# Kernel tuning notes

Hardware: AMD Instinct MI355X
Metric: run time of the kernel (lower is better)

The kernel has to match this reference:

```python
import jax, jax.numpy as jnp
import numpy as np

N_NODES = 100000
N_EDGES = 3200000
D = 128


def setup_inputs() -> dict:
    key = jax.random.key(0)
    k1, k2, k3, k4, k5 = jax.random.split(key, 5)
    x = jax.random.normal(k1, (N_NODES, D), dtype=jnp.float32)
    weight = jax.random.normal(k2, (D, D), dtype=jnp.float32) * (1.0 / np.sqrt(D))
    bias = jax.random.normal(k3, (D,), dtype=jnp.float32) * 0.01
    edge_weight = jax.random.uniform(k4, (N_EDGES,), dtype=jnp.float32)
    edge_index = jax.random.randint(k5, (2, N_EDGES), 0, N_NODES, dtype=jnp.int64 if jax.config.jax_enable_x64 else jnp.int32)
    return {"x": x, "weight": weight, "bias": bias,
            "edge_weight": edge_weight, "edge_index": edge_index}


def gcn_conv(x, weight, bias, edge_index, edge_weight):
    # PyG GCNConv defaults: normalize=True, add_self_loops=True (fill=1),
    # flow source_to_target: messages gathered from edge_index[0], scattered to edge_index[1].
    n = x.shape[0]
    src, dst = edge_index[0], edge_index[1]
    loop = jnp.arange(n, dtype=src.dtype)
    src = jnp.concatenate([src, loop])
    dst = jnp.concatenate([dst, loop])
    ew = jnp.concatenate([edge_weight, jnp.ones((n,), dtype=edge_weight.dtype)])
    deg = jax.ops.segment_sum(ew, dst, num_segments=n)          # [N]
    dinv = jnp.where(deg > 0, jax.lax.rsqrt(jnp.where(deg > 0, deg, 1.0)), 0.0)
    norm = dinv[src] * ew * dinv[dst]                           # [E+N]
    h = x @ weight.T                                            # [N, D_out]
    msg = h[src] * norm[:, None]                                # gather + scale
    out = jax.ops.segment_sum(msg, dst, num_segments=n)         # scatter-add
    return out + bias


def reference(x, weight, bias, edge_weight, edge_index):
    h = gcn_conv(x, weight, bias, edge_index, edge_weight)
    h = jax.nn.relu(h)            # normalizer is Identity, activation=F.relu
    h = h + x                     # input_dim == output_dim -> projection=Identity
    # dropout: eval mode (deterministic reference) -> no-op
    return h
```

## Files before the change

kernel.cpp:

```cpp
#include <hip/hip_runtime.h>

#define N_NODES 100000
#define N_EDGES 3200000
#define DIM 128

#define NB_C  98
#define CAP_C 36864
#define NB_F  1568
#define CAP_F 2560
#define CAP   96



__device__ __forceinline__ unsigned short f2bf(float f) {
    unsigned u = __float_as_uint(f);
    return (unsigned short)((u + 0x7fffu + ((u >> 16) & 1u)) >> 16);
}


__global__ __launch_bounds__(256) void zero_i_kernel(int* __restrict__ p, int n) {
    int i = blockIdx.x * 256 + threadIdx.x;
    if (i < n) p[i] = 0;
}

__global__ __launch_bounds__(256) void zero_f_kernel(float* __restrict__ p, int n) {
    int i = blockIdx.x * 256 + threadIdx.x;
    if (i < n) p[i] = 0.0f;
}

__global__ __launch_bounds__(256) void zero_u64_kernel(unsigned long long* __restrict__ p, int n) {
    int i = blockIdx.x * 256 + threadIdx.x;
    if (i < n) p[i] = 0ull;
}

__global__ __launch_bounds__(256) void zero_f4_kernel(float4* __restrict__ p, int n4) {
    int i = blockIdx.x * 256 + threadIdx.x;
    if (i < n4) p[i] = make_float4(0.f, 0.f, 0.f, 0.f);
}

__global__ __launch_bounds__(256) void dinv_kernel(float* __restrict__ deg) {
    int i = blockIdx.x * 256 + threadIdx.x;
    if (i < N_NODES) deg[i] = rsqrtf(deg[i] + 1.0f);
}

__global__ __launch_bounds__(256) void dinv_packed_kernel(const unsigned long long* __restrict__ packed,
                                                          float* __restrict__ dinv) {
    int i = blockIdx.x * 256 + threadIdx.x;
    if (i < N_NODES) {
        unsigned long long p = packed[i];
        float deg = (float)(p & 0xFFFFFFFFFFull) * (1.0f / 4294967296.0f);
        dinv[i] = rsqrtf(deg + 1.0f);
    }
}

__global__ __launch_bounds__(256) void wt_kernel(const float* __restrict__ W,
                                                 float* __restrict__ Wt) {
    int idx = blockIdx.x * 256 + threadIdx.x;
    int j = idx >> 7, k = idx & 127;
    Wt[k * 128 + j] = W[idx];
}


__global__ __launch_bounds__(256) void prep_kernel(const float* __restrict__ W,
                                                   float* __restrict__ Wt,
                                                   int* __restrict__ fills) {
    const int b = blockIdx.x;
    const int tid = threadIdx.x;
    if (b < 64) {
        int idx = b * 256 + tid;
        int j = idx >> 7, k = idx & 127;
        Wt[k * 128 + j] = W[idx];
    } else {
        int i = (b - 64) * 256 + tid;
        if (i < NB_C + NB_F) fills[i] = 0;
    }
}


__global__ __launch_bounds__(256) void partA1_kernel(const int* __restrict__ ei,
                                                     const float* __restrict__ ew,
                                                     int* __restrict__ fill_c,
                                                     unsigned long long* __restrict__ edc) {
    __shared__ int hist[NB_C];
    __shared__ int base[NB_C];
    const int tid = threadIdx.x;
    const int blockbase = blockIdx.x * 4096;
    for (int i = tid; i < NB_C; i += 256) hist[i] = 0;
    __syncthreads();

    unsigned long long pay[16];
    unsigned meta[16];
#pragma unroll
    for (int i = 0; i < 16; ++i) {
        int e = blockbase + i * 256 + tid;
        meta[i] = 0xFFFFFFFFu;
        if (e < N_EDGES) {
            int src = ei[e];
            int dst = ei[N_EDGES + e];
            float w = ew[e];
            int cb = dst >> 10;
            int pos = atomicAdd(&hist[cb], 1);
            pay[i] = ((unsigned long long)__float_as_uint(w) << 32)
                   | ((unsigned)(dst & 1023) << 17) | (unsigned)src;
            meta[i] = ((unsigned)cb << 16) | (unsigned)pos;
        }
    }
    __syncthreads();
    for (int c = tid; c < NB_C; c += 256) {
        int cnt = hist[c];
        base[c] = (cnt > 0) ? atomicAdd(&fill_c[c], cnt) : 0;
    }
    __syncthreads();
#pragma unroll
    for (int i = 0; i < 16; ++i) {
        if (meta[i] != 0xFFFFFFFFu) {
            int cb = (int)(meta[i] >> 16);
            int pos = base[cb] + (int)(meta[i] & 0xFFFFu);
            if (pos < CAP_C)
                edc[(unsigned)cb * CAP_C + (unsigned)pos] = pay[i];
        }
    }
}


__global__ __launch_bounds__(256) void partA2_kernel(const int* __restrict__ fill_c,
                                                     const unsigned long long* __restrict__ edc,
                                                     int* __restrict__ fill_f,
                                                     unsigned long long* __restrict__ edf) {
    __shared__ int hist[16];
    __shared__ int base[16];
    const int tid = threadIdx.x;
    const int cb = blockIdx.x / 9;
    const int lo = (blockIdx.x % 9) * 4096;
    const int cnt_c = min(fill_c[cb], CAP_C);
    const int hi = min(lo + 4096, cnt_c);
    if (tid < 16) hist[tid] = 0;
    __syncthreads();

    unsigned long long pay[16];
    unsigned meta[16];
#pragma unroll
    for (int i = 0; i < 16; ++i) {
        int idx = lo + i * 256 + tid;
        meta[i] = 0xFFFFFFFFu;
        if (idx < hi) {
            unsigned long long p = edc[(unsigned)cb * CAP_C + (unsigned)idx];
            int f = (int)((p >> 23) & 15);
            int pos = atomicAdd(&hist[f], 1);
            pay[i] = p;
            meta[i] = ((unsigned)f << 16) | (unsigned)pos;
        }
    }
    __syncthreads();
    if (tid < 16) {
        int c = hist[tid];
        base[tid] = (c > 0) ? atomicAdd(&fill_f[cb * 16 + tid], c) : 0;
    }
    __syncthreads();
#pragma unroll
    for (int i = 0; i < 16; ++i) {
        if (meta[i] != 0xFFFFFFFFu) {
            int f = (int)(meta[i] >> 16);
            int pos = base[f] + (int)(meta[i] & 0xFFFFu);
            if (pos < CAP_F)
                edf[((unsigned)(cb * 16 + f)) * CAP_F + (unsigned)pos] = pay[i];
        }
    }
}


__global__ __launch_bounds__(256) void partB_kernel(const int* __restrict__ fill_f,
                                                    unsigned long long* __restrict__ edf,
                                                    float* __restrict__ dinv,
                                                    int* __restrict__ row_start,
                                                    int* __restrict__ row_cnt,
                                                    const float4* __restrict__ x4,
                                                    ushort4* __restrict__ xh4) {
    __shared__ int hist[1024];
    __shared__ int pref[1024];
    __shared__ float degs[64];
    __shared__ int stripe[64];
    const int tid = threadIdx.x;
    const int fb = blockIdx.x;
    const int node_base = fb * 64;
    const int cnt = min(fill_f[fb], CAP_F);
    for (int i = tid; i < 1024; i += 256) hist[i] = 0;
    if (tid < 64) degs[tid] = 0.0f;
    __syncthreads();

    unsigned long long pay[10];
    unsigned meta[10];
    int m = 0;
    for (int idx = tid; idx < cnt; idx += 256) {
        unsigned long long p = edf[(unsigned)fb * CAP_F + (unsigned)idx];
        int dl = (int)((p >> 17) & 63);
        int src = (int)(p & 0x1FFFFull);
        int bin = dl * 16 + (src >> 13);
        int pos = atomicAdd(&hist[bin], 1);
        atomicAdd(&degs[dl], __uint_as_float((unsigned)(p >> 32)));
        pay[m] = p;
        meta[m] = ((unsigned)bin << 16) | (unsigned)pos;
        ++m;
    }
    __syncthreads();
    if (tid < 64) {
        int s = 0;
#pragma unroll
        for (int k = 0; k < 16; ++k) s += hist[tid * 16 + k];
        stripe[tid] = s;
    }
    __syncthreads();
    if (tid == 0) {
        int run = 0;
#pragma unroll
        for (int i = 0; i < 64; ++i) { int t = stripe[i]; stripe[i] = run; run += t; }
    }
    __syncthreads();
    if (tid < 64) {
        int run = stripe[tid];
#pragma unroll
        for (int k = 0; k < 16; ++k) { pref[tid * 16 + k] = run; run += hist[tid * 16 + k]; }
    }
    __syncthreads();
    if (tid < 64) {
        int node = node_base + tid;
        if (node < N_NODES) {
            float dv = rsqrtf(degs[tid] + 1.0f);
            dinv[node] = dv;
            degs[tid] = dv;
            int s0 = pref[tid * 16];
            int s1 = (tid < 63) ? pref[(tid + 1) * 16] : cnt;
            row_start[node] = fb * CAP_F + s0;
            row_cnt[node] = s1 - s0;
        }
    }
    for (int i = 0; i < m; ++i) {
        int bin = (int)(meta[i] >> 16);
        edf[(unsigned)fb * CAP_F + (unsigned)(pref[bin] + (int)(meta[i] & 0xFFFFu))] = pay[i];
    }
    __syncthreads();
#pragma unroll
    for (int i = 0; i < 8; ++i) {
        int idx = i * 256 + tid;
        int r = idx >> 5;
        int node = node_base + r;
        if (node < N_NODES) {
            float dv = degs[r];
            float4 v = x4[(unsigned)node * 32u + (unsigned)(idx & 31)];
            ushort4 h;
            h.x = f2bf(v.x * dv); h.y = f2bf(v.y * dv);
            h.z = f2bf(v.z * dv); h.w = f2bf(v.w * dv);
            xh4[(unsigned)node * 32u + (unsigned)(idx & 31)] = h;
        }
    }
}


__global__ __launch_bounds__(256) void gatherc_kernel(const int* __restrict__ row_start,
                                                      const int* __restrict__ row_cnt,
                                                      const unsigned long long* __restrict__ edf,
                                                      const float* __restrict__ dinv,
                                                      const unsigned* __restrict__ xh,
                                                      float2* __restrict__ agg2) {
    const int lane = threadIdx.x & 63;
    const int node = blockIdx.x * 4 + (threadIdx.x >> 6);

    const int cnt = row_cnt[node];
    const int start = row_start[node];
    float ax0 = 0.f, ay0 = 0.f, ax1 = 0.f, ay1 = 0.f;

    for (int b = 0; b < cnt; b += 64) {
        int idx = b + lane;
        const bool valid = idx < cnt;
        if (!valid) idx = cnt - 1;
        unsigned long long p = edf[(unsigned)(start + idx)];
        int msrc = (int)(p & 0x1FFFFull);
        float mw = valid ? __uint_as_float((unsigned)(p >> 32)) : 0.0f;
        const int mcnt = min(64, cnt - b);
        const int ng = (mcnt + 7) >> 3;

        unsigned va[8], vb[8];

#define PREF(buf, JB)                                                          \
        _Pragma("unroll")                                                      \
        for (int j = 0; j < 8; ++j) {                                          \
            int s = __builtin_amdgcn_readlane(msrc, (JB) + j);                 \
            buf[j] = xh[(unsigned)s * 64u + (unsigned)lane];                   \
        }
#define CONSUME(buf, JB)                                                       \
        _Pragma("unroll")                                                      \
        for (int j = 0; j < 8; ++j) {                                          \
            float w = __int_as_float(                                          \
                __builtin_amdgcn_readlane(__float_as_int(mw), (JB) + j));      \
            if (j & 1) {                                                       \
                ax1 = fmaf(__uint_as_float(buf[j] << 16), w, ax1);             \
                ay1 = fmaf(__uint_as_float(buf[j] & 0xffff0000u), w, ay1);     \
            } else {                                                           \
                ax0 = fmaf(__uint_as_float(buf[j] << 16), w, ax0);             \
                ay0 = fmaf(__uint_as_float(buf[j] & 0xffff0000u), w, ay0);     \
            }                                                                  \
        }

        PREF(va, 0);
        int g = 0;
        for (; g + 2 < ng; g += 2) {
            PREF(vb, (g + 1) * 8);
            CONSUME(va, g * 8);
            PREF(va, (g + 2) * 8);
            CONSUME(vb, (g + 1) * 8);
        }
        if (g + 1 < ng) {
            PREF(vb, (g + 1) * 8);
            CONSUME(va, g * 8);
            CONSUME(vb, (g + 1) * 8);
        } else {
            CONSUME(va, g * 8);
        }
#undef PREF
#undef CONSUME
    }

    float di = dinv[node];
    agg2[(unsigned)node * 64u + lane] = make_float2((ax0 + ax1) * di, (ay0 + ay1) * di);
}


__global__ __launch_bounds__(256) void bucket_f32_kernel(const int* __restrict__ ei,
                                                         const float* __restrict__ ew,
                                                         unsigned long long* __restrict__ packed,
                                                         int2* __restrict__ ed) {
    int e = blockIdx.x * 256 + threadIdx.x;
    int src = ei[e];
    int dst = ei[N_EDGES + e];
    float w = ew[e];
    unsigned long long inc = (1ull << 40) | (unsigned long long)(w * 4294967296.0f);
    unsigned long long old = atomicAdd(&packed[dst], inc);
    unsigned slot = (unsigned)(old >> 40);
    if (slot < CAP) {
        ed[(unsigned)dst * CAP + slot] = make_int2(src, __float_as_int(w));
    }
}

__global__ __launch_bounds__(256) void gatherb_f32_kernel(const unsigned long long* __restrict__ packed,
                                                          const int2* __restrict__ ed,
                                                          const float* __restrict__ dinv,
                                                          const float2* __restrict__ x2,
                                                          float2* __restrict__ agg2) {
    const int wave = threadIdx.x >> 6;
    const int lane = threadIdx.x & 63;
    const int node = blockIdx.x * 4 + wave;

    int cnt = (int)(packed[node] >> 40);
    cnt = min(cnt, CAP);
    const unsigned base = (unsigned)node * CAP;
    float2 acc = make_float2(0.f, 0.f);

    for (int b = 0; b < cnt; b += 64) {
        int idx = b + lane;
        if (idx >= cnt) idx = cnt - 1;
        int2 my = ed[base + idx];
        float wmy = __int_as_float(my.y) * dinv[my.x];
        int m = min(64, cnt - b);
#pragma unroll 8
        for (int j = 0; j < m; ++j) {
            int s = __builtin_amdgcn_readlane(my.x, j);
            float w = __int_as_float(__builtin_amdgcn_readlane(__float_as_int(wmy), j));
            float2 v = x2[(unsigned)s * 64u + lane];
            acc.x = fmaf(v.x, w, acc.x); acc.y = fmaf(v.y, w, acc.y);
        }
    }
    float di = dinv[node];
    acc.x *= di; acc.y *= di;
    agg2[(unsigned)node * 64u + lane] = acc;
}

__global__ __launch_bounds__(256) void count_deg_kernel(const int* __restrict__ ei,
                                                        const float* __restrict__ ew,
                                                        int* __restrict__ count,
                                                        float* __restrict__ deg) {
    int e = blockIdx.x * 256 + threadIdx.x;
    int dst = ei[N_EDGES + e];
    atomicAdd(&count[dst], 1);
    atomicAdd(&deg[dst], ew[e]);
}

__global__ __launch_bounds__(256) void scatter_kernel(const int* __restrict__ ei,
                                                      const float* __restrict__ ew,
                                                      const float* __restrict__ dinv,
                                                      const float4* __restrict__ x4,
                                                      float* __restrict__ agg) {
    unsigned gid = blockIdx.x * 256u + threadIdx.x;
    unsigned e  = gid >> 5;
    unsigned f4 = gid & 31u;
    int src = ei[e];
    int dst = ei[N_EDGES + e];
    float w = dinv[src] * ew[e] * dinv[dst];
    float4 v = x4[(unsigned)src * 32u + f4];
    float* o = agg + ((unsigned)dst * 128u + f4 * 4u);
    atomicAdd(o + 0, v.x * w);
    atomicAdd(o + 1, v.y * w);
    atomicAdd(o + 2, v.z * w);
    atomicAdd(o + 3, v.w * w);
}


__global__ __launch_bounds__(256) void final_kernel(const float* __restrict__ agg_in,
                                                    const float* __restrict__ x,
                                                    const float* __restrict__ bias,
                                                    const float* __restrict__ dinv,
                                                    const float* __restrict__ Wt,
                                                    float* __restrict__ out) {
    __shared__ float sh_wt[16384];
    const int tid = threadIdx.x;
    {
        const float4* s4 = (const float4*)Wt;
        float4* d4 = (float4*)sh_wt;
#pragma unroll
        for (int i = 0; i < 16; ++i) d4[i * 256 + tid] = s4[i * 256 + tid];
    }
    __syncthreads();

    const int wave = tid >> 6;
    const int lane = tid & 63;
    const int rowbase = blockIdx.x * 32 + wave * 8;

    float areg[16];
#pragma unroll
    for (int r = 0; r < 8; ++r) {
        int row = rowbase + r;
        float di = dinv[row];
        float di2 = di * di;
        int base = row * 128;
        areg[2 * r]     = agg_in[base + lane]      + x[base + lane]      * di2;
        areg[2 * r + 1] = agg_in[base + 64 + lane] + x[base + 64 + lane] * di2;
    }

    float acc0[8], acc1[8];
#pragma unroll
    for (int r = 0; r < 8; ++r) { acc0[r] = 0.f; acc1[r] = 0.f; }

    const float2* wt2 = (const float2*)sh_wt;

#pragma unroll
    for (int kh = 0; kh < 2; ++kh) {
#pragma unroll 16
        for (int kk = 0; kk < 64; ++kk) {
            int k = kh * 64 + kk;
            float2 w = wt2[k * 64 + lane];
#pragma unroll
            for (int r = 0; r < 8; ++r) {
                float ak = __uint_as_float(
                    __builtin_amdgcn_readlane(__float_as_uint(areg[2 * r + kh]), kk));
                acc0[r] = fmaf(ak, w.x, acc0[r]);
                acc1[r] = fmaf(ak, w.y, acc1[r]);
            }
        }
    }

    float2 b = ((const float2*)bias)[lane];
#pragma unroll
    for (int r = 0; r < 8; ++r) {
        int row = rowbase + r;
        float2 xr = ((const float2*)x)[row * 64 + lane];
        float v0 = fmaxf(acc0[r] + b.x, 0.f) + xr.x;
        float v1 = fmaxf(acc1[r] + b.y, 0.f) + xr.y;
        ((float2*)out)[row * 64 + lane] = make_float2(v0, v1);
    }
}


extern "C" void kernel_launch(void* const* d_in, const int* in_sizes, int n_in,
                              void* d_out, int out_size, void* d_ws, size_t ws_size,
                              hipStream_t stream) {
    const float* x    = (const float*)d_in[0];
    const float* W    = (const float*)d_in[1];
    const float* bias = (const float*)d_in[2];
    const float* ew   = (const float*)d_in[3];
    const int*   ei   = (const int*)d_in[4];
    float* out = (float*)d_out;
    char* ws = (char*)d_ws;

    unsigned short* xhA  = (unsigned short*)ws;
    float* WtA       = (float*)(ws + 25600000);
    float* dinvA     = (float*)(ws + 25665536);
    int*   row_start = (int*)  (ws + 26065536);
    int*   row_cnt   = (int*)  (ws + 26465536);
    int*   fill_c    = (int*)  (ws + 26865536);
    int*   fill_f    = fill_c + NB_C;
    unsigned long long* edc = (unsigned long long*)(ws + 26872256);
    unsigned long long* edf = (unsigned long long*)(ws + 55773632);
    const size_t WS_PART = 87886272ull;

    unsigned long long* packed = (unsigned long long*)ws;
    float* dinvB = (float*)(ws + 800000);
    float* WtB   = (float*)(ws + 1200000);
    int2*  edB   = (int2*)(ws + 1265536);
    const size_t WS_BUCKET = 1265536ull + (size_t)N_NODES * CAP * 8ull;

    if (ws_size >= WS_PART) {
        prep_kernel<<<71, 256, 0, stream>>>(W, WtA, fill_c);
        partA1_kernel<<<(N_EDGES + 4095) / 4096, 256, 0, stream>>>(ei, ew, fill_c, edc);
        partA2_kernel<<<NB_C * 9, 256, 0, stream>>>(fill_c, edc, fill_f, edf);
        partB_kernel<<<NB_F, 256, 0, stream>>>(fill_f, edf, dinvA, row_start, row_cnt,
                                               (const float4*)x, (ushort4*)xhA);
        gatherc_kernel<<<N_NODES / 4, 256, 0, stream>>>(row_start, row_cnt, edf, dinvA,
                                                        (const unsigned*)xhA, (float2*)out);
        final_kernel<<<N_NODES / 32, 256, 0, stream>>>(out, x, bias, dinvA, WtA, out);
    } else if (ws_size >= WS_BUCKET) {
        zero_u64_kernel<<<(N_NODES + 255) / 256, 256, 0, stream>>>(packed, N_NODES);
        wt_kernel<<<64, 256, 0, stream>>>(W, WtB);
        bucket_f32_kernel<<<N_EDGES / 256, 256, 0, stream>>>(ei, ew, packed, edB);
        dinv_packed_kernel<<<(N_NODES + 255) / 256, 256, 0, stream>>>(packed, dinvB);
        gatherb_f32_kernel<<<N_NODES / 4, 256, 0, stream>>>(packed, edB, dinvB,
                                                            (const float2*)x, (float2*)out);
        final_kernel<<<N_NODES / 32, 256, 0, stream>>>(out, x, bias, dinvB, WtB, out);
    } else {
        float* deg   = (float*)(ws);
        float* Wt    = (float*)(ws + 400000);
        int*   count = (int*)  (ws + 465536);
        zero_f_kernel<<<(N_NODES + 255) / 256, 256, 0, stream>>>(deg, N_NODES);
        zero_i_kernel<<<(N_NODES + 255) / 256, 256, 0, stream>>>(count, N_NODES);
        wt_kernel<<<64, 256, 0, stream>>>(W, Wt);
        zero_f4_kernel<<<(N_NODES * DIM / 4) / 256, 256, 0, stream>>>((float4*)out,
                                                                      N_NODES * DIM / 4);
        count_deg_kernel<<<N_EDGES / 256, 256, 0, stream>>>(ei, ew, count, deg);
        dinv_kernel<<<(N_NODES + 255) / 256, 256, 0, stream>>>(deg);
        scatter_kernel<<<(N_EDGES / 256) * 32, 256, 0, stream>>>(ei, ew, deg,
                                                                 (const float4*)x, out);
        final_kernel<<<N_NODES / 32, 256, 0, stream>>>(out, x, bias, deg, Wt, out);
    }
}
```

Baseline: 399.4 us.

## Use split-bf16 MFMA for final projection and simplify partB binning

Replaces the FP32 scalar final matmul with a kernel that splits both the aggregated activations and the weights into bf16 high and low parts. It then runs three bf16 MFMA products per tile to approximate FP32 accuracy. The weight is pre-swizzled in prep_kernel into the MFMA fragment layout. partB also drops the per-destination source sub-binning, which was a 1024-bin histogram, in favour of a 64-bin per-node histogram. This removes prefix-scan passes but may lose the gather locality that the source sorting gave. Precision drops slightly because the lo×lo term is omitted.

```diff
diff --git a/kernel.cpp b/kernel.cpp
--- a/kernel.cpp
+++ b/kernel.cpp
@@ -10,6 +10,9 @@
 #define CAP_F 2560
 #define CAP   96
 
+
+typedef __attribute__((ext_vector_type(4))) float f32x4;
+typedef __attribute__((ext_vector_type(8))) short s16x8;
 
 
 __device__ __forceinline__ unsigned short f2bf(float f) {
@@ -62,14 +65,24 @@
 
 
 __global__ __launch_bounds__(256) void prep_kernel(const float* __restrict__ W,
-                                                   float* __restrict__ Wt,
+                                                   ushort* __restrict__ wf_hi,
+                                                   ushort* __restrict__ wf_lo,
                                                    int* __restrict__ fills) {
     const int b = blockIdx.x;
     const int tid = threadIdx.x;
     if (b < 64) {
-        int idx = b * 256 + tid;
-        int j = idx >> 7, k = idx & 127;
-        Wt[k * 128 + j] = W[idx];
+        int idx  = b * 256 + tid;
+        int j    = idx & 7;
+        int lane = (idx >> 3) & 63;
+        int ks   = (idx >> 9) & 3;
+        int ct   = idx >> 11;
+        int col  = ct * 16 + (lane & 15);
+        int k    = ks * 32 + ((lane >> 4) << 3) + j;
+        float w  = W[col * 128 + k];
+        unsigned short hb = f2bf(w);
+        float rem = w - __uint_as_float((unsigned)hb << 16);
+        wf_hi[idx] = hb;
+        wf_lo[idx] = f2bf(rem);
     } else {
         int i = (b - 64) * 256 + tid;
         if (i < NB_C + NB_F) fills[i] = 0;
@@ -176,16 +189,14 @@
                                                     int* __restrict__ row_cnt,
                                                     const float4* __restrict__ x4,
                                                     ushort4* __restrict__ xh4) {
-    __shared__ int hist[1024];
-    __shared__ int pref[1024];
+    __shared__ int hist[64];
     __shared__ float degs[64];
-    __shared__ int stripe[64];
+    __shared__ int pref[64];
     const int tid = threadIdx.x;
     const int fb = blockIdx.x;
     const int node_base = fb * 64;
     const int cnt = min(fill_f[fb], CAP_F);
-    for (int i = tid; i < 1024; i += 256) hist[i] = 0;
-    if (tid < 64) degs[tid] = 0.0f;
+    if (tid < 64) { hist[tid] = 0; degs[tid] = 0.0f; }
     __syncthreads();
 
     unsigned long long pay[10];
@@ -194,32 +205,17 @@
     for (int idx = tid; idx < cnt; idx += 256) {
         unsigned long long p = edf[(unsigned)fb * CAP_F + (unsigned)idx];
         int dl = (int)((p >> 17) & 63);
-        int src = (int)(p & 0x1FFFFull);
-        int bin = dl * 16 + (src >> 13);
-        int pos = atomicAdd(&hist[bin], 1);
+        int pos = atomicAdd(&hist[dl], 1);
         atomicAdd(&degs[dl], __uint_as_float((unsigned)(p >> 32)));
         pay[m] = p;
-        meta[m] = ((unsigned)bin << 16) | (unsigned)pos;
+        meta[m] = ((unsigned)dl << 16) | (unsigned)pos;
         ++m;
-    }
-    __syncthreads();
-    if (tid < 64) {
-        int s = 0;
-#pragma unroll
-        for (int k = 0; k < 16; ++k) s += hist[tid * 16 + k];
-        stripe[tid] = s;
     }
     __syncthreads();
     if (tid == 0) {
         int run = 0;
 #pragma unroll
-        for (int i = 0; i < 64; ++i) { int t = stripe[i]; stripe[i] = run; run += t; }
-    }
-    __syncthreads();
-    if (tid < 64) {
-        int run = stripe[tid];
-#pragma unroll
-        for (int k = 0; k < 16; ++k) { pref[tid * 16 + k] = run; run += hist[tid * 16 + k]; }
+        for (int n = 0; n < 64; ++n) { pref[n] = run; run += hist[n]; }
     }
     __syncthreads();
     if (tid < 64) {
@@ -228,15 +224,13 @@
             float dv = rsqrtf(degs[tid] + 1.0f);
             dinv[node] = dv;
             degs[tid] = dv;
-            int s0 = pref[tid * 16];
-            int s1 = (tid < 63) ? pref[(tid + 1) * 16] : cnt;
-            row_start[node] = fb * CAP_F + s0;
-            row_cnt[node] = s1 - s0;
+            row_start[node] = fb * CAP_F + pref[tid];
+            row_cnt[node] = hist[tid];
         }
     }
     for (int i = 0; i < m; ++i) {
-        int bin = (int)(meta[i] >> 16);
-        edf[(unsigned)fb * CAP_F + (unsigned)(pref[bin] + (int)(meta[i] & 0xFFFFu))] = pay[i];
+        int dl = (int)(meta[i] >> 16);
+        edf[(unsigned)fb * CAP_F + (unsigned)(pref[dl] + (int)(meta[i] & 0xFFFFu))] = pay[i];
     }
     __syncthreads();
 #pragma unroll
@@ -404,6 +398,87 @@
 }
 
 
+__global__ __launch_bounds__(256) void final_mfma_kernel(const float* __restrict__ agg_in,
+                                                         const float* __restrict__ x,
+                                                         const float* __restrict__ bias,
+                                                         const float* __restrict__ dinv,
+                                                         const ushort* __restrict__ wf_hi,
+                                                         const ushort* __restrict__ wf_lo,
+                                                         float* __restrict__ out) {
+    __shared__ ushort sh_hi[16384];
+    __shared__ ushort sh_lo[16384];
+    const int tid = threadIdx.x;
+    {
+        const float4* sh4 = (const float4*)wf_hi;
+        const float4* sl4 = (const float4*)wf_lo;
+        float4* dh = (float4*)sh_hi;
+        float4* dl = (float4*)sh_lo;
+#pragma unroll
+        for (int i = 0; i < 8; ++i) {
+            dh[i * 256 + tid] = sh4[i * 256 + tid];
+            dl[i * 256 + tid] = sl4[i * 256 + tid];
+        }
+    }
+    __syncthreads();
+
+    const int wave = tid >> 6;
+    const int lane = tid & 63;
+    const int r0 = blockIdx.x * 64 + wave * 16;
+    const int mrow = lane & 15;
+    const int kg = lane >> 4;
+    const int arow = min(r0 + mrow, N_NODES - 1);
+    const float di = dinv[arow];
+    const float di2 = di * di;
+
+    s16x8 ah[4], al[4];
+#pragma unroll
+    for (int ks = 0; ks < 4; ++ks) {
+        const float* ap = agg_in + (unsigned)arow * 128u + ks * 32 + kg * 8;
+        const float* xp = x      + (unsigned)arow * 128u + ks * 32 + kg * 8;
+        float4 a0 = *(const float4*)ap;
+        float4 a1 = *(const float4*)(ap + 4);
+        float4 x0 = *(const float4*)xp;
+        float4 x1 = *(const float4*)(xp + 4);
+        float v[8] = {a0.x + x0.x * di2, a0.y + x0.y * di2,
+                      a0.z + x0.z * di2, a0.w + x0.w * di2,
+                      a1.x + x1.x * di2, a1.y + x1.y * di2,
+                      a1.z + x1.z * di2, a1.w + x1.w * di2};
+        s16x8 h, l;
+#pragma unroll
+        for (int j = 0; j < 8; ++j) {
+            unsigned short hb = f2bf(v[j]);
+            h[j] = (short)hb;
+            l[j] = (short)f2bf(v[j] - __uint_as_float((unsigned)hb << 16));
+        }
+        ah[ks] = h; al[ks] = l;
+    }
+
+#pragma unroll
+    for (int ct = 0; ct < 8; ++ct) {
+        f32x4 acc = {0.f, 0.f, 0.f, 0.f};
+#pragma unroll
+        for (int ks = 0; ks < 4; ++ks) {
+            const int fo = ((ct * 4 + ks) * 64 + lane) * 8;
+            s16x8 bh = *(const s16x8*)&sh_hi[fo];
+            s16x8 bl = *(const s16x8*)&sh_lo[fo];
+            acc = __builtin_amdgcn_mfma_f32_16x16x32_bf16(ah[ks], bh, acc, 0, 0, 0);
+            acc = __builtin_amdgcn_mfma_f32_16x16x32_bf16(ah[ks], bl, acc, 0, 0, 0);
+            acc = __builtin_amdgcn_mfma_f32_16x16x32_bf16(al[ks], bh, acc, 0, 0, 0);
+        }
+        const int col = ct * 16 + mrow;
+        const float bv = bias[col];
+#pragma unroll
+        for (int v = 0; v < 4; ++v) {
+            const int row = r0 + kg * 4 + v;
+            if (row < N_NODES) {
+                float o = fmaxf(acc[v] + bv, 0.f) + x[(unsigned)row * 128u + col];
+                out[(unsigned)row * 128u + col] = o;
+            }
+        }
+    }
+}
+
+
 __global__ __launch_bounds__(256) void final_kernel(const float* __restrict__ agg_in,
                                                     const float* __restrict__ x,
                                                     const float* __restrict__ bias,
@@ -481,7 +556,8 @@
     char* ws = (char*)d_ws;
 
     unsigned short* xhA  = (unsigned short*)ws;
-    float* WtA       = (float*)(ws + 25600000);
+    ushort* wfhi     = (ushort*)(ws + 25600000);
+    ushort* wflo     = wfhi + 16384;
     float* dinvA     = (float*)(ws + 25665536);
     int*   row_start = (int*)  (ws + 26065536);
     int*   row_cnt   = (int*)  (ws + 26465536);
@@ -498,14 +574,15 @@
     const size_t WS_BUCKET = 1265536ull + (size_t)N_NODES * CAP * 8ull;
 
     if (ws_size >= WS_PART) {
-        prep_kernel<<<71, 256, 0, stream>>>(W, WtA, fill_c);
+        prep_kernel<<<71, 256, 0, stream>>>(W, wfhi, wflo, fill_c);
         partA1_kernel<<<(N_EDGES + 4095) / 4096, 256, 0, stream>>>(ei, ew, fill_c, edc);
         partA2_kernel<<<NB_C * 9, 256, 0, stream>>>(fill_c, edc, fill_f, edf);
         partB_kernel<<<NB_F, 256, 0, stream>>>(fill_f, edf, dinvA, row_start, row_cnt,
                                                (const float4*)x, (ushort4*)xhA);
         gatherc_kernel<<<N_NODES / 4, 256, 0, stream>>>(row_start, row_cnt, edf, dinvA,
                                                         (const unsigned*)xhA, (float2*)out);
-        final_kernel<<<N_NODES / 32, 256, 0, stream>>>(out, x, bias, dinvA, WtA, out);
+        final_mfma_kernel<<<(N_NODES + 63) / 64, 256, 0, stream>>>(out, x, bias, dinvA,
+                                                                   wfhi, wflo, out);
     } else if (ws_size >= WS_BUCKET) {
         zero_u64_kernel<<<(N_NODES + 255) / 256, 256, 0, stream>>>(packed, N_NODES);
         wt_kernel<<<64, 256, 0, stream>>>(W, WtB);
```

Result: faster. 362.2 us (-9.3%).
